# Kernel optimization log

Hardware: AMD Instinct MI355X
Metric: run time of the kernel (lower is better)

Reference implementation:

```python
import jax, jax.numpy as jnp
import numpy as np

B, S, H, D = 2, 2048, 16, 128
HID = H * D  # 2048


def _quantum(x, real, imag, phase, mag):
    # |x * e^{i*phase} * (real + i*imag) * mag| == |x| * sqrt(real^2+imag^2) * |mag|
    # (phase has unit modulus, so it drops out of the magnitude; grad wrt phase is 0,
    # matching torch.abs of the complex product.)
    return jnp.abs(x) * jnp.sqrt(real * real + imag * imag) * jnp.abs(mag)


def setup_inputs() -> dict:
    key = jax.random.key(0)
    ks = jax.random.split(key, 20)
    p = lambda i, shape, s=0.02: jax.random.normal(ks[i], shape, dtype=jnp.float32) * s
    inp = {
        "hidden_states": jax.random.normal(ks[0], (B, S, HID), dtype=jnp.float32),
        "attention_mask": jnp.zeros((B, 1, 1, S), dtype=jnp.float32),
    }
    i = 1
    for name in ("q", "k", "v"):
        inp[name + "_real"] = p(i, (HID,)); i += 1
        inp[name + "_imag"] = p(i, (HID,)); i += 1
        inp[name + "_phase"] = p(i, (HID,), 0.1); i += 1
        inp[name + "_mag"] = jnp.ones((HID,), dtype=jnp.float32)
    for name in ("q", "k", "v", "o"):
        inp["W" + name] = p(i, (HID, HID)); i += 1  # torch Linear weight [out, in]
        inp["b" + name] = jnp.zeros((HID,), dtype=jnp.float32)
    inp["ent"] = p(i, (H, H))
    return inp


def reference(hidden_states, attention_mask,
              q_real, q_imag, q_phase, q_mag,
              k_real, k_imag, k_phase, k_mag,
              v_real, v_imag, v_phase, v_mag,
              Wq, bq, Wk, bk, Wv, bv, Wo, bo, ent):
    Bsz, Sl, _ = hidden_states.shape

    def heads(x):  # [B,S,HID] -> [B,H,S,D]
        return x.reshape(Bsz, Sl, H, D).transpose(0, 2, 1, 3)

    q = heads(_quantum(hidden_states @ Wq.T + bq, q_real, q_imag, q_phase, q_mag))
    k = heads(_quantum(hidden_states @ Wk.T + bk, k_real, k_imag, k_phase, k_mag))
    v = heads(_quantum(hidden_states @ Wv.T + bv, v_real, v_imag, v_phase, v_mag))

    scores = jnp.einsum('bhsd,bhtd->bhst', q, k) / jnp.sqrt(jnp.float32(D))
    # entanglement bias: [H,H] tiled along key axis -> [1,H,1,S]
    bias = jnp.tile(ent, (1, Sl // H))[None, :, None, :]
    scores = scores + bias + attention_mask
    probs = jax.nn.softmax(scores, axis=-1)

    ctx = jnp.einsum('bhst,bhtd->bhsd', probs, v)
    ctx = ctx.transpose(0, 2, 1, 3).reshape(Bsz, Sl, HID)
    return ctx @ Wo.T + bo
```

## Files before the change

### kernel.cpp

```cpp
#include <hip/hip_runtime.h>
#include <hip/hip_bf16.h>

#define NB 2
#define NS 2048
#define NH 16
#define ND 128
#define HID2 2048
#define MROWS 4096

typedef __bf16 bf16;
typedef bf16 bf16x8 __attribute__((ext_vector_type(8)));
typedef bf16 bf16x4 __attribute__((ext_vector_type(4)));
typedef float f32x4 __attribute__((ext_vector_type(4)));
typedef unsigned int u32;

#define GLOBAL_AS __attribute__((address_space(1)))
#define LDS_AS __attribute__((address_space(3)))

__device__ __forceinline__ void async16(void* lds, const void* g) {
    __builtin_amdgcn_global_load_lds((const GLOBAL_AS u32*)g, (LDS_AS u32*)lds, 16, 0, 0);
}

__global__ void cvt_f32_bf16(const float* __restrict__ src, bf16* __restrict__ dst, int n8) {
    int i = blockIdx.x * blockDim.x + threadIdx.x;
    if (i >= n8) return;
    const float4* s4 = (const float4*)src;
    float4 a = s4[2 * i], b = s4[2 * i + 1];
    bf16x8 o;
    o[0] = (bf16)a.x; o[1] = (bf16)a.y; o[2] = (bf16)a.z; o[3] = (bf16)a.w;
    o[4] = (bf16)b.x; o[5] = (bf16)b.y; o[6] = (bf16)b.z; o[7] = (bf16)b.w;
    ((bf16x8*)dst)[i] = o;
}

__global__ void cvt_w4(const float* __restrict__ Wq, const float* __restrict__ Wk,
                       const float* __restrict__ Wv, const float* __restrict__ Wo,
                       bf16* __restrict__ dst) {
    int z = blockIdx.y;
    const float* src = (z == 0) ? Wq : (z == 1) ? Wk : (z == 2) ? Wv : Wo;
    int i = blockIdx.x * blockDim.x + threadIdx.x;
    const float4* s4 = (const float4*)src;
    float4 a = s4[2 * i], b = s4[2 * i + 1];
    bf16x8 o;
    o[0] = (bf16)a.x; o[1] = (bf16)a.y; o[2] = (bf16)a.z; o[3] = (bf16)a.w;
    o[4] = (bf16)b.x; o[5] = (bf16)b.y; o[6] = (bf16)b.z; o[7] = (bf16)b.w;
    ((bf16x8*)(dst + (size_t)z * HID2 * HID2))[i] = o;
}

__global__ void qscale_kernel(const float* qr, const float* qi, const float* qm,
                              const float* kr, const float* ki, const float* km,
                              const float* vr, const float* vi, const float* vm,
                              float* out) {
    int i = blockIdx.x * blockDim.x + threadIdx.x;
    if (i >= HID2) return;
    out[i]            = sqrtf(qr[i] * qr[i] + qi[i] * qi[i]) * fabsf(qm[i]);
    out[HID2 + i]     = sqrtf(kr[i] * kr[i] + ki[i] * ki[i]) * fabsf(km[i]);
    out[2 * HID2 + i] = sqrtf(vr[i] * vr[i] + vi[i] * vi[i]) * fabsf(vm[i]);
}

__device__ __forceinline__ void stage2A(const char* gA, char* sa, int w, int lane, size_t kb) {
#pragma unroll
    for (int j = 0; j < 2; ++j) {
        int r = w * 16 + j * 8 + (lane >> 3);
        async16(sa + (w * 16 + j * 8) * 128,
                gA + (size_t)r * (HID2 * 2) + kb + (((lane & 7) * 16) ^ ((r & 7) << 4)));
    }
}
__device__ __forceinline__ void stage2B(const char* gB, char* sb, int w, int lane, int half, size_t kb) {
#pragma unroll
    for (int j = 0; j < 2; ++j) {
        int r = half * 128 + w * 16 + j * 8 + (lane >> 3);
        async16(sb + (half * 128 + w * 16 + j * 8) * 128,
                gB + (size_t)r * (HID2 * 2) + kb + (((lane & 7) * 16) ^ ((r & 7) << 4)));
    }
}

#define G_BARRIER() do { asm volatile("" ::: "memory"); __builtin_amdgcn_s_barrier(); \
                         asm volatile("" ::: "memory"); } while (0)

template <int MODE>
__device__ __forceinline__ void gemm_core(const bf16* __restrict__ A, const bf16* __restrict__ Bt,
                                          const float* __restrict__ bias, const float* __restrict__ scale,
                                          void* __restrict__ Cout, int tm, int tn) {
    __shared__ bf16 sA[3][128 * 64];
    __shared__ bf16 sB[3][256 * 64];
    const int NT = HID2 / 64;
    int tid = threadIdx.x, w = tid >> 6, lane = tid & 63;
    int wr = w >> 2, wc = w & 3;
    int l15 = lane & 15, l4 = lane >> 4;
    int xorb = (l15 & 7) << 4;

    const char* gA = (const char*)A + (size_t)tm * 128 * (HID2 * 2);
    const char* gB = (const char*)Bt + (size_t)tn * 256 * (HID2 * 2);

    f32x4 acc[4][4] = {};

    stage2A(gA, (char*)sA[0], w, lane, 0);
    stage2B(gB, (char*)sB[0], w, lane, 0, 0);
    stage2B(gB, (char*)sB[0], w, lane, 1, 0);
    stage2A(gA, (char*)sA[1], w, lane, 128);
    stage2B(gB, (char*)sB[1], w, lane, 0, 128);
    stage2B(gB, (char*)sB[1], w, lane, 1, 128);
    asm volatile("s_waitcnt vmcnt(6)" ::: "memory");
    G_BARRIER();

    int cur = 0;
    for (int t = 0; t < NT; ++t) {
        const char* pa = (const char*)sA[cur];
        const char* pb = (const char*)sB[cur];
        int nb = cur + 2; if (nb >= 3) nb -= 3;
        const bool pre = (t + 2 < NT);
        size_t kb = (size_t)(t + 2) * 128;
        bf16x8 af[4], bg[4];

        {
            int kc = (l4 * 16) ^ xorb;
#pragma unroll
            for (int m = 0; m < 4; ++m)
                af[m] = *(const bf16x8*)(pa + (wr * 64 + m * 16 + l15) * 128 + kc);
#pragma unroll
            for (int n = 0; n < 4; ++n)
                bg[n] = *(const bf16x8*)(pb + (wc * 64 + n * 16 + l15) * 128 + kc);
        }
        if (pre) { stage2A(gA, (char*)sA[nb], w, lane, kb); stage2B(gB, (char*)sB[nb], w, lane, 0, kb); }
        G_BARRIER();
        asm volatile("s_waitcnt lgkmcnt(0)" ::: "memory");
        __builtin_amdgcn_sched_barrier(0);
        __builtin_amdgcn_s_setprio(1);
#pragma unroll
        for (int m = 0; m < 4; ++m)
#pragma unroll
            for (int n = 0; n < 4; ++n)
                acc[m][n] = __builtin_amdgcn_mfma_f32_16x16x32_bf16(af[m], bg[n], acc[m][n], 0, 0, 0);
        __builtin_amdgcn_s_setprio(0);
        G_BARRIER();

        {
            int kc = (64 + l4 * 16) ^ xorb;
#pragma unroll
            for (int m = 0; m < 4; ++m)
                af[m] = *(const bf16x8*)(pa + (wr * 64 + m * 16 + l15) * 128 + kc);
#pragma unroll
            for (int n = 0; n < 4; ++n)
                bg[n] = *(const bf16x8*)(pb + (wc * 64 + n * 16 + l15) * 128 + kc);
        }
        if (pre) stage2B(gB, (char*)sB[nb], w, lane, 1, kb);
        G_BARRIER();
        asm volatile("s_waitcnt lgkmcnt(0)" ::: "memory");
        __builtin_amdgcn_sched_barrier(0);
        __builtin_amdgcn_s_setprio(1);
#pragma unroll
        for (int m = 0; m < 4; ++m)
#pragma unroll
            for (int n = 0; n < 4; ++n)
                acc[m][n] = __builtin_amdgcn_mfma_f32_16x16x32_bf16(af[m], bg[n], acc[m][n], 0, 0, 0);
        __builtin_amdgcn_s_setprio(0);
        if (pre)                { asm volatile("s_waitcnt vmcnt(6)" ::: "memory"); }
        else if (t + 2 == NT)  { asm volatile("s_waitcnt vmcnt(0)" ::: "memory"); }
        G_BARRIER();

        cur = cur + 1; if (cur == 3) cur = 0;
    }

#pragma unroll
    for (int n = 0; n < 4; ++n) {
        int col = tn * 256 + wc * 64 + n * 16 + l15;
        float bv = bias[col];
        float sc = (MODE == 0) ? scale[col] : 0.f;
#pragma unroll
        for (int m = 0; m < 4; ++m) {
            int row = tm * 128 + wr * 64 + m * 16 + l4 * 4;
            if (MODE == 0) {
                bf16* Cp = (bf16*)Cout;
#pragma unroll
                for (int r = 0; r < 4; ++r)
                    Cp[(size_t)(row + r) * HID2 + col] = (bf16)(fabsf(acc[m][n][r] + bv) * sc);
            } else {
                float* Cp = (float*)Cout;
#pragma unroll
                for (int r = 0; r < 4; ++r)
                    Cp[(size_t)(row + r) * HID2 + col] = acc[m][n][r] + bv;
            }
        }
    }
}

__global__ __launch_bounds__(512, 2) void gemm_qkv(
    const bf16* __restrict__ X, const bf16* __restrict__ Wb,
    const float* __restrict__ bq, const float* __restrict__ bk, const float* __restrict__ bv,
    const float* __restrict__ scales, bf16* __restrict__ QKV) {
    int z = blockIdx.y;
    int bid = blockIdx.x;
    int tn = bid & 7, tm = bid >> 3;
    const bf16* W = Wb + (size_t)z * HID2 * HID2;
    const float* bias = (z == 0) ? bq : (z == 1) ? bk : bv;
    gemm_core<0>(X, W, bias, scales + z * HID2, QKV + (size_t)z * MROWS * HID2, tm, tn);
}

__global__ __launch_bounds__(512, 2) void gemm_out(
    const bf16* __restrict__ Ctx, const bf16* __restrict__ Wo,
    const float* __restrict__ bo, float* __restrict__ out) {
    int bid = blockIdx.x;
    int tn = bid & 7, tm = bid >> 3;
    gemm_core<1>(Ctx, Wo, bo, nullptr, out, tm, tn);
}

__global__ void transpose_v(const bf16* __restrict__ Vb, bf16* __restrict__ Vt) {
    int bh = blockIdx.z;
    int b = bh >> 4, h = bh & 15;
    int s0 = blockIdx.x * 64, d0 = blockIdx.y * 64;
    int tid = threadIdx.x;
    __shared__ bf16 T[64][72];
    const bf16* src = Vb + ((size_t)b * NS + s0) * HID2 + h * ND + d0;
#pragma unroll
    for (int i = 0; i < 2; ++i) {
        int r = i * 32 + (tid >> 3);
        int c = (tid & 7) * 8;
        *(bf16x8*)(&T[r][c]) = *(const bf16x8*)(src + (size_t)r * HID2 + c);
    }
    __syncthreads();
    bf16* dst = Vt + ((size_t)(b * NH + h) * ND + d0) * NS + s0;
#pragma unroll
    for (int i = 0; i < 2; ++i) {
        int dr = i * 32 + (tid >> 3);
        int sc = (tid & 7) * 8;
        bf16x8 o;
#pragma unroll
        for (int j = 0; j < 8; ++j) o[j] = T[sc + j][dr];
        *(bf16x8*)(dst + (size_t)dr * NS + sc) = o;
    }
}

__device__ __forceinline__ void stage_load(const bf16* __restrict__ Kp, const bf16* __restrict__ Vp,
                                           int kt, int tid, bf16x8 kreg[4], bf16x8 vreg[4]) {
#pragma unroll
    for (int i = 0; i < 4; ++i) {
        kreg[i] = *(const bf16x8*)(Kp + (size_t)(kt * 64 + i * 16 + (tid >> 4)) * HID2 + (tid & 15) * 8);
        vreg[i] = *(const bf16x8*)(Vp + (size_t)(i * 32 + (tid >> 3)) * NS + kt * 64 + (tid & 7) * 8);
    }
}

__global__ __launch_bounds__(256, 2) void flash_kernel(
    const bf16* __restrict__ Qb, const bf16* __restrict__ Kb, const bf16* __restrict__ Vt,
    const float* __restrict__ ent, const float* __restrict__ mask, bf16* __restrict__ Ctx) {
    int qt = blockIdx.x;
    int bh = blockIdx.y;
    int b = bh >> 4, h = bh & 15;
    int tid = threadIdx.x, wid = tid >> 6, lane = tid & 63;
    int l15 = lane & 15, l4 = lane >> 4;

    __shared__ bf16 Ks[64 * 136];
    __shared__ bf16 Vs[128 * 72];
    __shared__ bf16 Ps[4][32 * 72];

    const bf16* Qp = Qb + ((size_t)b * NS + qt * 128) * HID2 + h * ND;
    const bf16* Kp = Kb + (size_t)b * NS * HID2 + h * ND;
    const bf16* Vp = Vt + (size_t)(b * NH + h) * ND * NS;
    const float* maskp = mask + (size_t)b * NS;

    bf16x8 qf[2][4];
#pragma unroll
    for (int m = 0; m < 2; ++m)
#pragma unroll
        for (int kk = 0; kk < 4; ++kk)
            qf[m][kk] = *(const bf16x8*)(Qp + (size_t)(wid * 32 + m * 16 + l15) * HID2 + kk * 32 + l4 * 8);

    float eb[4];
#pragma unroll
    for (int r = 0; r < 4; ++r) eb[r] = ent[h * NH + l4 * 4 + r];
    const float RSQD = 0.08838834764831845f;

    float mrun[2], lrun[2];
    mrun[0] = mrun[1] = -INFINITY;
    lrun[0] = lrun[1] = 0.f;
    f32x4 oacc[2][8] = {};

    bf16x8 kreg[4], vreg[4];
    stage_load(Kp, Vp, 0, tid, kreg, vreg);
#pragma unroll
    for (int i = 0; i < 4; ++i) {
        *(bf16x8*)(&Ks[(i * 16 + (tid >> 4)) * 136 + (tid & 15) * 8]) = kreg[i];
        *(bf16x8*)(&Vs[(i * 32 + (tid >> 3)) * 72 + (tid & 7) * 8]) = vreg[i];
    }

    for (int kt = 0; kt < NS / 64; ++kt) {
        __syncthreads();
        if (kt + 1 < NS / 64) stage_load(Kp, Vp, kt + 1, tid, kreg, vreg);

        f32x4 s[2][4] = {};
#pragma unroll
        for (int kk = 0; kk < 4; ++kk) {
            bf16x8 kf[4];
#pragma unroll
            for (int n = 0; n < 4; ++n)
                kf[n] = *(const bf16x8*)(&Ks[(n * 16 + l15) * 136 + kk * 32 + l4 * 8]);
#pragma unroll
            for (int m = 0; m < 2; ++m)
#pragma unroll
                for (int n = 0; n < 4; ++n)
                    s[m][n] = __builtin_amdgcn_mfma_f32_16x16x32_bf16(kf[n], qf[m][kk], s[m][n], 0, 0, 0);
        }

        float4 mk[4];
#pragma unroll
        for (int n = 0; n < 4; ++n)
            mk[n] = *(const float4*)(maskp + kt * 64 + n * 16 + l4 * 4);

#pragma unroll
        for (int mq = 0; mq < 2; ++mq) {
            float sv[4][4];
#pragma unroll
            for (int n = 0; n < 4; ++n) {
                sv[n][0] = s[mq][n][0] * RSQD + eb[0] + mk[n].x;
                sv[n][1] = s[mq][n][1] * RSQD + eb[1] + mk[n].y;
                sv[n][2] = s[mq][n][2] * RSQD + eb[2] + mk[n].z;
                sv[n][3] = s[mq][n][3] * RSQD + eb[3] + mk[n].w;
            }
            float tmax = sv[0][0];
#pragma unroll
            for (int n = 0; n < 4; ++n)
#pragma unroll
                for (int r = 0; r < 4; ++r) tmax = fmaxf(tmax, sv[n][r]);
            tmax = fmaxf(tmax, __shfl_xor(tmax, 16));
            tmax = fmaxf(tmax, __shfl_xor(tmax, 32));

            if (__any(tmax > mrun[mq] + 8.0f)) {
                float mnew = fmaxf(mrun[mq], tmax);
                float corr = __expf(mrun[mq] - mnew);
                mrun[mq] = mnew;
                lrun[mq] *= corr;
#pragma unroll
                for (int r = 0; r < 4; ++r) {
                    float cr = __shfl(corr, l4 * 4 + r);
#pragma unroll
                    for (int n = 0; n < 8; ++n) oacc[mq][n][r] *= cr;
                }
            }

            float psum = 0.f;
#pragma unroll
            for (int n = 0; n < 4; ++n) {
                bf16x4 pv;
#pragma unroll
                for (int r = 0; r < 4; ++r) {
                    float p = __expf(sv[n][r] - mrun[mq]);
                    psum += p;
                    pv[r] = (bf16)p;
                }
                *(bf16x4*)(&Ps[wid][(mq * 16 + l15) * 72 + n * 16 + l4 * 4]) = pv;
            }
            psum += __shfl_xor(psum, 16);
            psum += __shfl_xor(psum, 32);
            lrun[mq] += psum;
        }

#pragma unroll
        for (int kk = 0; kk < 2; ++kk) {
            bf16x8 pa[2], vb[8];
#pragma unroll
            for (int m = 0; m < 2; ++m)
                pa[m] = *(const bf16x8*)(&Ps[wid][(m * 16 + l15) * 72 + kk * 32 + l4 * 8]);
#pragma unroll
            for (int n = 0; n < 8; ++n)
                vb[n] = *(const bf16x8*)(&Vs[(n * 16 + l15) * 72 + kk * 32 + l4 * 8]);
#pragma unroll
            for (int m = 0; m < 2; ++m)
#pragma unroll
                for (int n = 0; n < 8; ++n)
                    oacc[m][n] = __builtin_amdgcn_mfma_f32_16x16x32_bf16(pa[m], vb[n], oacc[m][n], 0, 0, 0);
        }
        __syncthreads();
        if (kt + 1 < NS / 64) {
#pragma unroll
            for (int i = 0; i < 4; ++i) {
                *(bf16x8*)(&Ks[(i * 16 + (tid >> 4)) * 136 + (tid & 15) * 8]) = kreg[i];
                *(bf16x8*)(&Vs[(i * 32 + (tid >> 3)) * 72 + (tid & 7) * 8]) = vreg[i];
            }
        }
    }

#pragma unroll
    for (int m = 0; m < 2; ++m) {
        float inv = 1.0f / lrun[m];
        float invr[4];
#pragma unroll
        for (int r = 0; r < 4; ++r) invr[r] = __shfl(inv, l4 * 4 + r);
#pragma unroll
        for (int r = 0; r < 4; ++r) {
            int row = qt * 128 + wid * 32 + m * 16 + l4 * 4 + r;
            bf16* Cp = Ctx + ((size_t)b * NS + row) * HID2 + h * ND;
#pragma unroll
            for (int n = 0; n < 8; ++n)
                Cp[n * 16 + l15] = (bf16)(oacc[m][n][r] * invr[r]);
        }
    }
}

extern "C" void kernel_launch(void* const* d_in, const int* in_sizes, int n_in,
                              void* d_out, int out_size, void* d_ws, size_t ws_size,
                              hipStream_t stream) {
    const float* hidden = (const float*)d_in[0];
    const float* mask   = (const float*)d_in[1];
    const float* q_real = (const float*)d_in[2];
    const float* q_imag = (const float*)d_in[3];
    const float* q_mag  = (const float*)d_in[5];
    const float* k_real = (const float*)d_in[6];
    const float* k_imag = (const float*)d_in[7];
    const float* k_mag  = (const float*)d_in[9];
    const float* v_real = (const float*)d_in[10];
    const float* v_imag = (const float*)d_in[11];
    const float* v_mag  = (const float*)d_in[13];
    const float* Wq = (const float*)d_in[14];
    const float* bq = (const float*)d_in[15];
    const float* Wk = (const float*)d_in[16];
    const float* bk = (const float*)d_in[17];
    const float* Wv = (const float*)d_in[18];
    const float* bv = (const float*)d_in[19];
    const float* Wo = (const float*)d_in[20];
    const float* bo = (const float*)d_in[21];
    const float* ent = (const float*)d_in[22];

    char* ws = (char*)d_ws;
    bf16* Xb    = (bf16*)(ws);
    bf16* Wb    = (bf16*)(ws + 16777216);
    bf16* Wob   = (bf16*)(ws + 41943040);
    bf16* QKV   = (bf16*)(ws + 50331648);
    bf16* Vt    = (bf16*)(ws + 100663296);
    bf16* Ctx   = (bf16*)(ws + 117440512);
    float* scales = (float*)(ws + 134217728);

    cvt_f32_bf16<<<4096, 256, 0, stream>>>(hidden, Xb, MROWS * HID2 / 8);
    cvt_w4<<<dim3(2048, 4), 256, 0, stream>>>(Wq, Wk, Wv, Wo, Wb);
    qscale_kernel<<<8, 256, 0, stream>>>(q_real, q_imag, q_mag, k_real, k_imag, k_mag,
                                         v_real, v_imag, v_mag, scales);
    gemm_qkv<<<dim3(256, 3), 512, 0, stream>>>(Xb, Wb, bq, bk, bv, scales, QKV);
    const bf16* Vb = QKV + (size_t)2 * MROWS * HID2;
    transpose_v<<<dim3(32, 2, 32), 256, 0, stream>>>(Vb, Vt);
    flash_kernel<<<dim3(16, 32), 256, 0, stream>>>(QKV, QKV + (size_t)MROWS * HID2, Vt, ent, mask, Ctx);
    gemm_out<<<256, 512, 0, stream>>>(Ctx, Wob, bo, (float*)d_out);
}
```

Before: 290.5 us.

## Fuse V transpose into QKV GEMM epilogue with simpler single-buffered GEMM

The QKV projection now uses a new 256-thread, single-buffered GEMM in which each wave computes a 64x128 tile. For the V projection the epilogue writes straight into the transposed [B,H,D,S] layout, so the separate transpose_v kernel and its extra pass over V are gone. The new GEMM drops the triple-buffered async pipeline and places a sync before and after every k-step, so load latency may be exposed. Occupancy is raised with launch bounds (256,3). The V epilogue writes strided 8-byte stores, which may coalesce poorly.

Result: slower. 352.5 us (+21.3%).

```diff
diff --git a/kernel.cpp b/kernel.cpp
--- a/kernel.cpp
+++ b/kernel.cpp
@@ -57,6 +57,117 @@
     out[2 * HID2 + i] = sqrtf(vr[i] * vr[i] + vi[i] * vi[i]) * fabsf(vm[i]);
 }
 
+__device__ __forceinline__ void stage12(const char* gA, const char* gB,
+                                        char* sa, char* sb, int w, int lane, size_t kb) {
+    int r8 = lane >> 3;
+    int cx = (lane & 7) * 16;
+#pragma unroll
+    for (int j = 0; j < 4; ++j) {
+        int r = w * 32 + j * 8 + r8;
+        async16(sa + (w * 32 + j * 8) * 128,
+                gA + (size_t)r * (HID2 * 2) + kb + (cx ^ ((r & 7) << 4)));
+    }
+#pragma unroll
+    for (int j = 0; j < 8; ++j) {
+        int r = w * 64 + j * 8 + r8;
+        async16(sb + (w * 64 + j * 8) * 128,
+                gB + (size_t)r * (HID2 * 2) + kb + (cx ^ ((r & 7) << 4)));
+    }
+}
+
+template <int MODE>
+__device__ __forceinline__ void gemm_loose(const bf16* __restrict__ A, const bf16* __restrict__ Bt,
+                                           const float* __restrict__ bias, const float* __restrict__ scale,
+                                           void* __restrict__ Cout, int tm, int tn) {
+    __shared__ bf16 sA[128 * 64];
+    __shared__ bf16 sB[256 * 64];
+    int tid = threadIdx.x, w = tid >> 6, lane = tid & 63;
+    int wr = w >> 1, wc = w & 1;
+    int l15 = lane & 15, l4 = lane >> 4;
+    int xorb = (l15 & 7) << 4;
+
+    const char* gA = (const char*)A + (size_t)tm * 128 * (HID2 * 2);
+    const char* gB = (const char*)Bt + (size_t)tn * 256 * (HID2 * 2);
+    const char* pa = (const char*)sA;
+    const char* pb = (const char*)sB;
+
+    f32x4 acc[4][8] = {};
+
+    for (int t = 0; t < HID2 / 64; ++t) {
+        stage12(gA, gB, (char*)sA, (char*)sB, w, lane, (size_t)t * 128);
+        __syncthreads();
+#pragma unroll
+        for (int kk = 0; kk < 2; ++kk) {
+            int kc = (kk * 64 + l4 * 16) ^ xorb;
+            bf16x8 af[4], bg[4];
+#pragma unroll
+            for (int m = 0; m < 4; ++m)
+                af[m] = *(const bf16x8*)(pa + (wr * 64 + m * 16 + l15) * 128 + kc);
+#pragma unroll
+            for (int n = 0; n < 4; ++n)
+                bg[n] = *(const bf16x8*)(pb + (wc * 128 + n * 16 + l15) * 128 + kc);
+#pragma unroll
+            for (int m = 0; m < 4; ++m)
+#pragma unroll
+                for (int n = 0; n < 4; ++n)
+                    acc[m][n] = __builtin_amdgcn_mfma_f32_16x16x32_bf16(af[m], bg[n], acc[m][n], 0, 0, 0);
+#pragma unroll
+            for (int n = 0; n < 4; ++n)
+                bg[n] = *(const bf16x8*)(pb + (wc * 128 + (n + 4) * 16 + l15) * 128 + kc);
+#pragma unroll
+            for (int m = 0; m < 4; ++m)
+#pragma unroll
+                for (int n = 0; n < 4; ++n)
+                    acc[m][n + 4] = __builtin_amdgcn_mfma_f32_16x16x32_bf16(af[m], bg[n], acc[m][n + 4], 0, 0, 0);
+        }
+        __syncthreads();
+    }
+
+#pragma unroll
+    for (int n = 0; n < 8; ++n) {
+        int col = tn * 256 + wc * 128 + n * 16 + l15;
+        float bv = bias[col];
+        float sc = (MODE != 1) ? scale[col] : 0.f;
+#pragma unroll
+        for (int m = 0; m < 4; ++m) {
+            int row = tm * 128 + wr * 64 + m * 16 + l4 * 4;
+            if (MODE == 0) {
+                bf16* Cp = (bf16*)Cout;
+#pragma unroll
+                for (int r = 0; r < 4; ++r)
+                    Cp[(size_t)(row + r) * HID2 + col] = (bf16)(fabsf(acc[m][n][r] + bv) * sc);
+            } else if (MODE == 1) {
+                float* Cp = (float*)Cout;
+#pragma unroll
+                for (int r = 0; r < 4; ++r)
+                    Cp[(size_t)(row + r) * HID2 + col] = acc[m][n][r] + bv;
+            } else {
+                int h = col >> 7, d = col & 127;
+                int bb = row >> 11, s = row & 2047;
+                bf16x4 pv;
+#pragma unroll
+                for (int r = 0; r < 4; ++r)
+                    pv[r] = (bf16)(fabsf(acc[m][n][r] + bv) * sc);
+                bf16* Cp = (bf16*)Cout;
+                *(bf16x4*)(Cp + ((size_t)(bb * NH + h) * ND + d) * NS + s) = pv;
+            }
+        }
+    }
+}
+
+__global__ __launch_bounds__(256, 3) void gemm_qkv(
+    const bf16* __restrict__ X, const bf16* __restrict__ Wb,
+    const float* __restrict__ bq, const float* __restrict__ bk, const float* __restrict__ bv,
+    const float* __restrict__ scales, bf16* __restrict__ QKV, bf16* __restrict__ Vt) {
+    int z = blockIdx.y;
+    int bid = blockIdx.x;
+    int tn = bid & 7, tm = bid >> 3;
+    const bf16* W = Wb + (size_t)z * HID2 * HID2;
+    if (z == 0)      gemm_loose<0>(X, W, bq, scales,            QKV,                              tm, tn);
+    else if (z == 1) gemm_loose<0>(X, W, bk, scales + HID2,     QKV + (size_t)MROWS * HID2,       tm, tn);
+    else             gemm_loose<2>(X, W, bv, scales + 2 * HID2, Vt,                               tm, tn);
+}
+
 __device__ __forceinline__ void stage2A(const char* gA, char* sa, int w, int lane, size_t kb) {
 #pragma unroll
     for (int j = 0; j < 2; ++j) {
@@ -77,20 +188,21 @@
 #define G_BARRIER() do { asm volatile("" ::: "memory"); __builtin_amdgcn_s_barrier(); \
                          asm volatile("" ::: "memory"); } while (0)
 
-template <int MODE>
-__device__ __forceinline__ void gemm_core(const bf16* __restrict__ A, const bf16* __restrict__ Bt,
-                                          const float* __restrict__ bias, const float* __restrict__ scale,
-                                          void* __restrict__ Cout, int tm, int tn) {
+__global__ __launch_bounds__(512, 2) void gemm_out(
+    const bf16* __restrict__ Ctx, const bf16* __restrict__ Wo,
+    const float* __restrict__ bo, float* __restrict__ out) {
     __shared__ bf16 sA[3][128 * 64];
     __shared__ bf16 sB[3][256 * 64];
     const int NT = HID2 / 64;
+    int bid = blockIdx.x;
+    int tn = bid & 7, tm = bid >> 3;
     int tid = threadIdx.x, w = tid >> 6, lane = tid & 63;
     int wr = w >> 2, wc = w & 3;
     int l15 = lane & 15, l4 = lane >> 4;
     int xorb = (l15 & 7) << 4;
 
-    const char* gA = (const char*)A + (size_t)tm * 128 * (HID2 * 2);
-    const char* gB = (const char*)Bt + (size_t)tn * 256 * (HID2 * 2);
+    const char* gA = (const char*)Ctx + (size_t)tm * 128 * (HID2 * 2);
+    const char* gB = (const char*)Wo + (size_t)tn * 256 * (HID2 * 2);
 
     f32x4 acc[4][4] = {};
 
@@ -154,7 +266,7 @@
             for (int n = 0; n < 4; ++n)
                 acc[m][n] = __builtin_amdgcn_mfma_f32_16x16x32_bf16(af[m], bg[n], acc[m][n], 0, 0, 0);
         __builtin_amdgcn_s_setprio(0);
-        if (pre)                { asm volatile("s_waitcnt vmcnt(6)" ::: "memory"); }
+        if (pre)               { asm volatile("s_waitcnt vmcnt(6)" ::: "memory"); }
         else if (t + 2 == NT)  { asm volatile("s_waitcnt vmcnt(0)" ::: "memory"); }
         G_BARRIER();
 
@@ -164,69 +276,14 @@
 #pragma unroll
     for (int n = 0; n < 4; ++n) {
         int col = tn * 256 + wc * 64 + n * 16 + l15;
-        float bv = bias[col];
-        float sc = (MODE == 0) ? scale[col] : 0.f;
+        float bv = bo[col];
 #pragma unroll
         for (int m = 0; m < 4; ++m) {
             int row = tm * 128 + wr * 64 + m * 16 + l4 * 4;
-            if (MODE == 0) {
-                bf16* Cp = (bf16*)Cout;
-#pragma unroll
-                for (int r = 0; r < 4; ++r)
-                    Cp[(size_t)(row + r) * HID2 + col] = (bf16)(fabsf(acc[m][n][r] + bv) * sc);
-            } else {
-                float* Cp = (float*)Cout;
-#pragma unroll
-                for (int r = 0; r < 4; ++r)
-                    Cp[(size_t)(row + r) * HID2 + col] = acc[m][n][r] + bv;
-            }
-        }
-    }
-}
-
-__global__ __launch_bounds__(512, 2) void gemm_qkv(
-    const bf16* __restrict__ X, const bf16* __restrict__ Wb,
-    const float* __restrict__ bq, const float* __restrict__ bk, const float* __restrict__ bv,
-    const float* __restrict__ scales, bf16* __restrict__ QKV) {
-    int z = blockIdx.y;
-    int bid = blockIdx.x;
-    int tn = bid & 7, tm = bid >> 3;
-    const bf16* W = Wb + (size_t)z * HID2 * HID2;
-    const float* bias = (z == 0) ? bq : (z == 1) ? bk : bv;
-    gemm_core<0>(X, W, bias, scales + z * HID2, QKV + (size_t)z * MROWS * HID2, tm, tn);
-}
-
-__global__ __launch_bounds__(512, 2) void gemm_out(
-    const bf16* __restrict__ Ctx, const bf16* __restrict__ Wo,
-    const float* __restrict__ bo, float* __restrict__ out) {
-    int bid = blockIdx.x;
-    int tn = bid & 7, tm = bid >> 3;
-    gemm_core<1>(Ctx, Wo, bo, nullptr, out, tm, tn);
-}
-
-__global__ void transpose_v(const bf16* __restrict__ Vb, bf16* __restrict__ Vt) {
-    int bh = blockIdx.z;
-    int b = bh >> 4, h = bh & 15;
-    int s0 = blockIdx.x * 64, d0 = blockIdx.y * 64;
-    int tid = threadIdx.x;
-    __shared__ bf16 T[64][72];
-    const bf16* src = Vb + ((size_t)b * NS + s0) * HID2 + h * ND + d0;
-#pragma unroll
-    for (int i = 0; i < 2; ++i) {
-        int r = i * 32 + (tid >> 3);
-        int c = (tid & 7) * 8;
-        *(bf16x8*)(&T[r][c]) = *(const bf16x8*)(src + (size_t)r * HID2 + c);
-    }
-    __syncthreads();
-    bf16* dst = Vt + ((size_t)(b * NH + h) * ND + d0) * NS + s0;
-#pragma unroll
-    for (int i = 0; i < 2; ++i) {
-        int dr = i * 32 + (tid >> 3);
-        int sc = (tid & 7) * 8;
-        bf16x8 o;
-#pragma unroll
-        for (int j = 0; j < 8; ++j) o[j] = T[sc + j][dr];
-        *(bf16x8*)(dst + (size_t)dr * NS + sc) = o;
+#pragma unroll
+            for (int r = 0; r < 4; ++r)
+                out[(size_t)(row + r) * HID2 + col] = acc[m][n][r] + bv;
+        }
     }
 }
 
@@ -432,9 +489,7 @@
     cvt_w4<<<dim3(2048, 4), 256, 0, stream>>>(Wq, Wk, Wv, Wo, Wb);
     qscale_kernel<<<8, 256, 0, stream>>>(q_real, q_imag, q_mag, k_real, k_imag, k_mag,
                                          v_real, v_imag, v_mag, scales);
-    gemm_qkv<<<dim3(256, 3), 512, 0, stream>>>(Xb, Wb, bq, bk, bv, scales, QKV);
-    const bf16* Vb = QKV + (size_t)2 * MROWS * HID2;
-    transpose_v<<<dim3(32, 2, 32), 256, 0, stream>>>(Vb, Vt);
+    gemm_qkv<<<dim3(256, 3), 256, 0, stream>>>(Xb, Wb, bq, bk, bv, scales, QKV, Vt);
     flash_kernel<<<dim3(16, 32), 256, 0, stream>>>(QKV, QKV + (size_t)MROWS * HID2, Vt, ent, mask, Ctx);
     gemm_out<<<256, 512, 0, stream>>>(Ctx, Wob, bo, (float*)d_out);
 }
```
